# Kernel tuning notes

Hardware: AMD Instinct MI355X
Metric: run time of the kernel (lower is better)

The kernel has to match this reference:

```python
import jax, jax.numpy as jnp
import numpy as np
from jax import lax

WIRES = 4
EPS = 1e-5


def _conv2d(x, w, b):
    # x: [B,C,H,W], w: [O,I,3,3], SAME padding, stride 1
    y = lax.conv_general_dilated(x, w, (1, 1), 'SAME',
                                 dimension_numbers=('NCHW', 'OIHW', 'NCHW'))
    return y + b[None, :, None, None]


def _maxpool2(x):
    return lax.reduce_window(x, -jnp.inf, lax.max, (1, 1, 2, 2), (1, 1, 2, 2), 'VALID')


def _cnot_perm(c, t, n=WIRES):
    # wire 0 = most significant bit; CNOT is a self-inverse basis permutation
    idx = np.arange(2 ** n)
    cbit = (idx >> (n - 1 - c)) & 1
    flipped = idx ^ (1 << (n - 1 - t))
    return np.where(cbit == 1, flipped, idx)


_CNOT_PERMS = [_cnot_perm(c, c + 1) for c in range(WIRES - 1)]
_Z_SIGNS = np.stack([1.0 - 2.0 * ((np.arange(2 ** WIRES) >> (WIRES - 1 - i)) & 1)
                     for i in range(WIRES)], axis=1).astype(np.float32)  # [16, 4]


def _quantum_circuit(q_params, feats):
    # Batched state-vector sim of: RY(feats[i]) wire i; RX(params[i]) wire i;
    # CNOT chain; <Z_i>.  feats: [B,4], q_params: [4]
    hf = 0.5 * feats
    hp = 0.5 * q_params
    cy, sy = jnp.cos(hf), jnp.sin(hf)            # [B,4]
    cx, sx = jnp.cos(hp), jnp.sin(hp)            # [4]
    # per-wire state after RX @ RY |0>: amplitudes of |0>, |1>
    a0 = (cx * cy - 1j * sx * sy).astype(jnp.complex64)  # [B,4]
    a1 = (cx * sy - 1j * sx * cy).astype(jnp.complex64)  # [B,4]
    single = jnp.stack([a0, a1], axis=-1)        # [B,4,2]
    # product state -> full 16-dim state via successive outer products
    psi = single[:, 0]                           # [B,2]
    for i in range(1, WIRES):
        psi = (psi[:, :, None] * single[:, i][:, None, :]).reshape(psi.shape[0], -1)
    # CNOT chain = fixed basis permutations
    for perm in _CNOT_PERMS:
        psi = psi[:, perm]                       # [B,16]
    probs = psi.real ** 2 + psi.imag ** 2        # [B,16]
    return probs @ jnp.asarray(_Z_SIGNS)         # [B,4]


def setup_inputs() -> dict:
    key = jax.random.key(0)
    ks = jax.random.split(key, 8)
    B, C, H, W = 512, 1, 128, 128
    return {
        'x': jax.random.normal(ks[0], (B, C, H, W), jnp.float32),
        'conv1_w': jax.random.normal(ks[1], (8, C, 3, 3), jnp.float32) * 0.1,
        'conv1_b': jnp.zeros((8,), jnp.float32),
        'conv2_w': jax.random.normal(ks[2], (16, 8, 3, 3), jnp.float32) * 0.1,
        'conv2_b': jnp.zeros((16,), jnp.float32),
        'q_params': jax.random.normal(ks[3], (WIRES,), jnp.float32),
        'bn_gamma': jnp.ones((4,), jnp.float32),
        'bn_beta': jnp.zeros((4,), jnp.float32),
        'head_w': jax.random.normal(ks[4], (4, WIRES), jnp.float32) * 0.5,
        'head_b': jnp.zeros((4,), jnp.float32),
    }


def reference(x, conv1_w, conv1_b, conv2_w, conv2_b, q_params,
              bn_gamma, bn_beta, head_w, head_b):
    h = jax.nn.relu(_conv2d(x, conv1_w, conv1_b))
    h = _maxpool2(h)
    h = jax.nn.relu(_conv2d(h, conv2_w, conv2_b))
    h = _maxpool2(h)
    feats = h.mean(axis=(2, 3))                  # AdaptiveAvgPool2d(1) -> [B,16]
    q_out = _quantum_circuit(q_params, feats[:, :WIRES])  # [B,4]
    # BatchNorm1d (training mode, biased variance)
    mu = q_out.mean(axis=0)
    var = q_out.var(axis=0)
    normed = bn_gamma * (q_out - mu) / jnp.sqrt(var + EPS) + bn_beta
    return normed @ head_w.T + head_b
```

## Files before the change

### kernel.cpp

```cpp
#include <hip/hip_runtime.h>

#define EPS 1e-5f

typedef float f2 __attribute__((ext_vector_type(2)));
typedef float f4 __attribute__((ext_vector_type(4)));

__device__ __forceinline__ float uload(const float* __restrict__ p) {
  return __int_as_float(__builtin_amdgcn_readfirstlane(__float_as_int(*p)));
}

__device__ __forceinline__ f2 fma2(f2 a, f2 b, f2 c) {
  return __builtin_elementwise_fma(a, b, c);
}
__device__ __forceinline__ f2 splat2(float s) { f2 r; r.x = s; r.y = s; return r; }

__global__ __launch_bounds__(256, 4) void k12_fused(
    const float* __restrict__ x, const float* __restrict__ w1,
    const float* __restrict__ b1, const float* __restrict__ w2,
    const float* __restrict__ b2, float* __restrict__ partials) {
  __shared__ __align__(16) float p1[8][18][66];
  __shared__ float wred[4][4];

  const int q   = blockIdx.x & 3;
  const int b   = blockIdx.x >> 2;
  const int tid = threadIdx.x;
  const float* xb = x + (size_t)b * (128 * 128);

  auto c1_load = [&](int pos, float xin[4][6]) {
    const int gl = pos >> 5, i = pos & 31;
    const int G  = 16 * q - 1 + gl;
    const bool vG = ((unsigned)G) < 64u;
    const int xr0 = 2 * G - 1;
#pragma unroll
    for (int r = 0; r < 4; ++r) {
      const int row  = xr0 + r;
      const bool rok = vG && ((unsigned)row < 128u);
      const int rowc = min(max(row, 0), 127);
      const float* rp = xb + rowc * 128;
      const float le = rp[(i == 0) ? 0 : (4 * i - 1)];
      const f4 mid   = *(const f4*)(rp + 4 * i);
      const float ri = rp[(i == 31) ? 127 : (4 * i + 4)];
      xin[r][0] = (rok && i != 0)  ? le    : 0.f;
      xin[r][1] = rok              ? mid.x : 0.f;
      xin[r][2] = rok              ? mid.y : 0.f;
      xin[r][3] = rok              ? mid.z : 0.f;
      xin[r][4] = rok              ? mid.w : 0.f;
      xin[r][5] = (rok && i != 31) ? ri    : 0.f;
    }
  };
  auto c1_compute = [&](int pos, const float xin[4][6]) {
    const int gl = pos >> 5, i = pos & 31;
    const int G  = 16 * q - 1 + gl;
    const bool vG = ((unsigned)G) < 64u;
#pragma unroll 1
    for (int g = 0; g < 2; ++g) {
      f2 wpx[9][2], bias[2];
#pragma unroll
      for (int k = 0; k < 9; ++k)
#pragma unroll
        for (int p = 0; p < 2; ++p) {
          const int oc = 4 * g + 2 * p;
          f2 wv;
          wv.x = w1[oc * 9 + k];
          wv.y = w1[(oc + 1) * 9 + k];
          wpx[k][p] = wv;
        }
      bias[0].x = b1[4 * g];     bias[0].y = b1[4 * g + 1];
      bias[1].x = b1[4 * g + 2]; bias[1].y = b1[4 * g + 3];
#pragma unroll
      for (int p = 0; p < 2; ++p)
#pragma unroll
        for (int h = 0; h < 2; ++h) {
          f2 best = splat2(0.f);
#pragma unroll
          for (int dy = 0; dy < 2; ++dy)
#pragma unroll
            for (int dx = 0; dx < 2; ++dx) {
              f2 a = bias[p];
#pragma unroll
              for (int ky = 0; ky < 3; ++ky)
#pragma unroll
                for (int kx = 0; kx < 3; ++kx)
                  a = fma2(wpx[ky * 3 + kx][p],
                           splat2(xin[dy + ky][2 * h + dx + kx]), a);
              best.x = fmaxf(best.x, a.x);
              best.y = fmaxf(best.y, a.y);
            }
          const int oc0 = 4 * g + 2 * p;
          p1[oc0][gl][2 * i + 1 + h]     = vG ? best.x : 0.f;
          p1[oc0 + 1][gl][2 * i + 1 + h] = vG ? best.y : 0.f;
        }
    }
  };

  if (tid >= 96 && tid < 240) {
    int t = tid - 96;
    int ic = t / 18, r = t % 18;
    p1[ic][r][0]  = 0.f;
    p1[ic][r][65] = 0.f;
  }

  {
    float xin0[4][6];
    c1_load(tid, xin0);
    c1_compute(tid, xin0);
  }
#pragma unroll 1
  for (int pos = tid + 256; pos < 576; pos += 256) {
    float xin[4][6];
    c1_load(pos, xin);
    c1_compute(pos, xin);
  }
  __syncthreads();

  const int px2  = tid & 31;
  const int py2l = tid >> 5;

  f2 acc[2][2][2];
  {
    f2 bias0, bias1;
    bias0.x = b2[0]; bias0.y = b2[1];
    bias1.x = b2[2]; bias1.y = b2[3];
    acc[0][0][0] = bias0; acc[0][0][1] = bias0;
    acc[0][1][0] = bias0; acc[0][1][1] = bias0;
    acc[1][0][0] = bias1; acc[1][0][1] = bias1;
    acc[1][1][0] = bias1; acc[1][1][1] = bias1;
  }

  auto ld_xin = [&](int ic, float xin[4][4]) {
#pragma unroll
    for (int r = 0; r < 4; ++r) {
      const f2* rp = (const f2*)&p1[ic][2 * py2l + r][2 * px2];
      f2 v0 = rp[0], v1 = rp[1];
      xin[r][0] = v0.x; xin[r][1] = v0.y; xin[r][2] = v1.x; xin[r][3] = v1.y;
    }
  };
  auto c2_acc = [&](int ic, const float xin[4][4]) {
#pragma unroll
    for (int ky = 0; ky < 3; ++ky)
#pragma unroll
      for (int kx = 0; kx < 3; ++kx) {
        const int k = ky * 3 + kx;
        f2 wA, wB;
        wA.x = w2[0 * 72 + ic * 9 + k];
        wA.y = w2[1 * 72 + ic * 9 + k];
        wB.x = w2[2 * 72 + ic * 9 + k];
        wB.y = w2[3 * 72 + ic * 9 + k];
#pragma unroll
        for (int dy = 0; dy < 2; ++dy)
#pragma unroll
          for (int dx = 0; dx < 2; ++dx) {
            const f2 xs = splat2(xin[dy + ky][dx + kx]);
            acc[0][dy][dx] = fma2(wA, xs, acc[0][dy][dx]);
            acc[1][dy][dx] = fma2(wB, xs, acc[1][dy][dx]);
          }
      }
  };

  float xina[4][4], xinb[4][4];
  ld_xin(0, xina);
#pragma unroll 1
  for (int ic = 0; ic < 8; ic += 2) {
    ld_xin(ic + 1, xinb);
    c2_acc(ic, xina);
    if (ic < 6) ld_xin(ic + 2, xina);
    c2_acc(ic + 1, xinb);
  }

  const int lane = tid & 63, w = tid >> 6;
#pragma unroll
  for (int p = 0; p < 2; ++p) {
    f2 m01;
    m01.x = fmaxf(fmaxf(fmaxf(acc[p][0][0].x, acc[p][0][1].x),
                        fmaxf(acc[p][1][0].x, acc[p][1][1].x)), 0.f);
    m01.y = fmaxf(fmaxf(fmaxf(acc[p][0][0].y, acc[p][0][1].y),
                        fmaxf(acc[p][1][0].y, acc[p][1][1].y)), 0.f);
#pragma unroll
    for (int off = 32; off > 0; off >>= 1) {
      m01.x += __shfl_down(m01.x, off);
      m01.y += __shfl_down(m01.y, off);
    }
    if (lane == 0) { wred[w][2 * p] = m01.x; wred[w][2 * p + 1] = m01.y; }
  }
  __syncthreads();
  if (tid < 4) {
    float s = wred[0][tid] + wred[1][tid] + wred[2][tid] + wred[3][tid];
    partials[((size_t)b * 4 + q) * 4 + tid] = s;
  }
}

__global__ __launch_bounds__(512) void k3_tail(
    const float* __restrict__ partials, const float* __restrict__ qp,
    const float* __restrict__ gamma, const float* __restrict__ beta,
    const float* __restrict__ hw, const float* __restrict__ hb,
    float* __restrict__ out) {
  __shared__ float wsum[8][8];
  __shared__ float stats[8];
  const int tid = threadIdx.x;

  const f4* pp = (const f4*)(partials + tid * 16);
  f4 s0 = pp[0], s1 = pp[1], s2 = pp[2], s3 = pp[3];
  float f[4];
  f[0] = (s0.x + s1.x + s2.x + s3.x) * (1.f / 1024.f);
  f[1] = (s0.y + s1.y + s2.y + s3.y) * (1.f / 1024.f);
  f[2] = (s0.z + s1.z + s2.z + s3.z) * (1.f / 1024.f);
  f[3] = (s0.w + s1.w + s2.w + s3.w) * (1.f / 1024.f);

  float a0r[4], a0i[4], a1r[4], a1i[4];
#pragma unroll
  for (int i = 0; i < 4; ++i) {
    float cy, sy, cx, sx;
    __sincosf(0.5f * f[i], &sy, &cy);
    __sincosf(0.5f * uload(qp + i), &sx, &cx);
    a0r[i] = cx * cy; a0i[i] = -sx * sy;
    a1r[i] = cx * sy; a1i[i] = -sx * cy;
  }

  float pr[16], pi[16];
#pragma unroll
  for (int j = 0; j < 16; ++j) {
    float rr = 1.f, ii = 0.f;
#pragma unroll
    for (int w = 0; w < 4; ++w) {
      int bit = (j >> (3 - w)) & 1;
      float ar = bit ? a1r[w] : a0r[w];
      float ai = bit ? a1i[w] : a0i[w];
      float t = rr * ar - ii * ai;
      ii = rr * ai + ii * ar;
      rr = t;
    }
    pr[j] = rr; pi[j] = ii;
  }

  constexpr int comp[16] = {0, 1, 3, 2, 6, 7, 5, 4, 12, 13, 15, 14, 10, 11, 9, 8};
  float qv[4] = {0.f, 0.f, 0.f, 0.f};
#pragma unroll
  for (int j = 0; j < 16; ++j) {
    int s = comp[j];
    float p = pr[s] * pr[s] + pi[s] * pi[s];
#pragma unroll
    for (int i = 0; i < 4; ++i)
      qv[i] += ((j >> (3 - i)) & 1) ? -p : p;
  }

  float v[8];
#pragma unroll
  for (int i = 0; i < 4; ++i) { v[i] = qv[i]; v[4 + i] = qv[i] * qv[i]; }
#pragma unroll
  for (int k = 0; k < 8; ++k)
#pragma unroll
    for (int off = 32; off > 0; off >>= 1) v[k] += __shfl_down(v[k], off);
  const int lane = tid & 63, w = tid >> 6;
  if (lane == 0) {
#pragma unroll
    for (int k = 0; k < 8; ++k) wsum[w][k] = v[k];
  }
  __syncthreads();
  if (tid < 8) {
    float s = 0.f;
#pragma unroll
    for (int ww = 0; ww < 8; ++ww) s += wsum[ww][tid];
    stats[tid] = s * (1.f / 512.f);
  }
  __syncthreads();

  float nm[4];
#pragma unroll
  for (int i = 0; i < 4; ++i) {
    float mu  = stats[i];
    float var = stats[4 + i] - mu * mu;
    nm[i] = uload(gamma + i) * (qv[i] - mu) * rsqrtf(var + EPS) + uload(beta + i);
  }
#pragma unroll
  for (int k = 0; k < 4; ++k) {
    float o = uload(hb + k);
#pragma unroll
    for (int i = 0; i < 4; ++i) o = fmaf(nm[i], uload(hw + k * 4 + i), o);
    out[tid * 4 + k] = o;
  }
}

extern "C" void kernel_launch(void* const* d_in, const int* in_sizes, int n_in,
                              void* d_out, int out_size, void* d_ws, size_t ws_size,
                              hipStream_t stream) {
  const float* x  = (const float*)d_in[0];
  const float* w1 = (const float*)d_in[1];
  const float* b1 = (const float*)d_in[2];
  const float* w2 = (const float*)d_in[3];
  const float* b2 = (const float*)d_in[4];
  const float* qp = (const float*)d_in[5];
  const float* gm = (const float*)d_in[6];
  const float* bt = (const float*)d_in[7];
  const float* hw = (const float*)d_in[8];
  const float* hb = (const float*)d_in[9];
  float* out = (float*)d_out;

  float* partials = (float*)d_ws;

  k12_fused<<<512 * 4, 256, 0, stream>>>(x, w1, b1, w2, b2, partials);
  k3_tail<<<1, 512, 0, stream>>>(partials, qp, gm, bt, hw, hb, out);
}
```

Measured before the change: 117.9 us.

## Widen fused conv block to 576 threads and split conv2 channels across thread groups

The fused conv kernel now launches 576 threads per block, so each thread computes exactly one conv1 position with no second loop pass. For conv2, 512 threads are split into two groups of 256, each handling two output channels instead of four per thread, which halves per-thread accumulators and work. This adds parallelism and shortens per-thread serial work. The trade-off is larger blocks, 64 idle threads during conv2, and possibly lower occupancy now that the launch-bounds minimum-blocks hint is gone. It also reads redundant conv1 inputs.

```diff
diff --git a/kernel.cpp b/kernel.cpp
--- a/kernel.cpp
+++ b/kernel.cpp
@@ -14,12 +14,12 @@
 }
 __device__ __forceinline__ f2 splat2(float s) { f2 r; r.x = s; r.y = s; return r; }
 
-__global__ __launch_bounds__(256, 4) void k12_fused(
+__global__ __launch_bounds__(576) void k12_fused(
     const float* __restrict__ x, const float* __restrict__ w1,
     const float* __restrict__ b1, const float* __restrict__ w2,
     const float* __restrict__ b2, float* __restrict__ partials) {
   __shared__ __align__(16) float p1[8][18][66];
-  __shared__ float wred[4][4];
+  __shared__ float wred[8][2];
 
   const int q   = blockIdx.x & 3;
   const int b   = blockIdx.x >> 2;
@@ -93,6 +93,9 @@
     }
   };
 
+  float xin0[4][6];
+  c1_load(tid, xin0);
+
   if (tid >= 96 && tid < 240) {
     int t = tid - 96;
     int ic = t / 18, r = t % 18;
@@ -100,91 +103,76 @@
     p1[ic][r][65] = 0.f;
   }
 
-  {
-    float xin0[4][6];
-    c1_load(tid, xin0);
-    c1_compute(tid, xin0);
-  }
+  c1_compute(tid, xin0);
+  __syncthreads();
+
+  const int lane = tid & 63, w = tid >> 6;
+  if (tid < 512) {
+    const int px2  = tid & 31;
+    const int py2l = (tid >> 5) & 7;
+    const int g2 = __builtin_amdgcn_readfirstlane(tid >> 8);
+
+    f2 acc[2][2];
+    {
+      f2 bias;
+      bias.x = b2[2 * g2];
+      bias.y = b2[2 * g2 + 1];
+      acc[0][0] = bias; acc[0][1] = bias;
+      acc[1][0] = bias; acc[1][1] = bias;
+    }
+
+    auto ld_xin = [&](int ic, float xin[4][4]) {
+#pragma unroll
+      for (int r = 0; r < 4; ++r) {
+        const f2* rp = (const f2*)&p1[ic][2 * py2l + r][2 * px2];
+        f2 v0 = rp[0], v1 = rp[1];
+        xin[r][0] = v0.x; xin[r][1] = v0.y; xin[r][2] = v1.x; xin[r][3] = v1.y;
+      }
+    };
+    auto c2_acc = [&](int ic, const float xin[4][4]) {
+#pragma unroll
+      for (int ky = 0; ky < 3; ++ky)
+#pragma unroll
+        for (int kx = 0; kx < 3; ++kx) {
+          const int k = ky * 3 + kx;
+          f2 wp;
+          wp.x = w2[(2 * g2) * 72 + ic * 9 + k];
+          wp.y = w2[(2 * g2 + 1) * 72 + ic * 9 + k];
+#pragma unroll
+          for (int dy = 0; dy < 2; ++dy)
+#pragma unroll
+            for (int dx = 0; dx < 2; ++dx)
+              acc[dy][dx] = fma2(wp, splat2(xin[dy + ky][dx + kx]), acc[dy][dx]);
+        }
+    };
+
+    float xina[4][4], xinb[4][4];
+    ld_xin(0, xina);
 #pragma unroll 1
-  for (int pos = tid + 256; pos < 576; pos += 256) {
-    float xin[4][6];
-    c1_load(pos, xin);
-    c1_compute(pos, xin);
-  }
-  __syncthreads();
-
-  const int px2  = tid & 31;
-  const int py2l = tid >> 5;
-
-  f2 acc[2][2][2];
-  {
-    f2 bias0, bias1;
-    bias0.x = b2[0]; bias0.y = b2[1];
-    bias1.x = b2[2]; bias1.y = b2[3];
-    acc[0][0][0] = bias0; acc[0][0][1] = bias0;
-    acc[0][1][0] = bias0; acc[0][1][1] = bias0;
-    acc[1][0][0] = bias1; acc[1][0][1] = bias1;
-    acc[1][1][0] = bias1; acc[1][1][1] = bias1;
-  }
-
-  auto ld_xin = [&](int ic, float xin[4][4]) {
-#pragma unroll
-    for (int r = 0; r < 4; ++r) {
-      const f2* rp = (const f2*)&p1[ic][2 * py2l + r][2 * px2];
-      f2 v0 = rp[0], v1 = rp[1];
-      xin[r][0] = v0.x; xin[r][1] = v0.y; xin[r][2] = v1.x; xin[r][3] = v1.y;
-    }
-  };
-  auto c2_acc = [&](int ic, const float xin[4][4]) {
-#pragma unroll
-    for (int ky = 0; ky < 3; ++ky)
-#pragma unroll
-      for (int kx = 0; kx < 3; ++kx) {
-        const int k = ky * 3 + kx;
-        f2 wA, wB;
-        wA.x = w2[0 * 72 + ic * 9 + k];
-        wA.y = w2[1 * 72 + ic * 9 + k];
-        wB.x = w2[2 * 72 + ic * 9 + k];
-        wB.y = w2[3 * 72 + ic * 9 + k];
-#pragma unroll
-        for (int dy = 0; dy < 2; ++dy)
-#pragma unroll
-          for (int dx = 0; dx < 2; ++dx) {
-            const f2 xs = splat2(xin[dy + ky][dx + kx]);
-            acc[0][dy][dx] = fma2(wA, xs, acc[0][dy][dx]);
-            acc[1][dy][dx] = fma2(wB, xs, acc[1][dy][dx]);
-          }
-      }
-  };
-
-  float xina[4][4], xinb[4][4];
-  ld_xin(0, xina);
-#pragma unroll 1
-  for (int ic = 0; ic < 8; ic += 2) {
-    ld_xin(ic + 1, xinb);
-    c2_acc(ic, xina);
-    if (ic < 6) ld_xin(ic + 2, xina);
-    c2_acc(ic + 1, xinb);
-  }
-
-  const int lane = tid & 63, w = tid >> 6;
-#pragma unroll
-  for (int p = 0; p < 2; ++p) {
+    for (int ic = 0; ic < 8; ic += 2) {
+      ld_xin(ic + 1, xinb);
+      c2_acc(ic, xina);
+      if (ic < 6) ld_xin(ic + 2, xina);
+      c2_acc(ic + 1, xinb);
+    }
+
     f2 m01;
-    m01.x = fmaxf(fmaxf(fmaxf(acc[p][0][0].x, acc[p][0][1].x),
-                        fmaxf(acc[p][1][0].x, acc[p][1][1].x)), 0.f);
-    m01.y = fmaxf(fmaxf(fmaxf(acc[p][0][0].y, acc[p][0][1].y),
-                        fmaxf(acc[p][1][0].y, acc[p][1][1].y)), 0.f);
+    m01.x = fmaxf(fmaxf(fmaxf(acc[0][0].x, acc[0][1].x),
+                        fmaxf(acc[1][0].x, acc[1][1].x)), 0.f);
+    m01.y = fmaxf(fmaxf(fmaxf(acc[0][0].y, acc[0][1].y),
+                        fmaxf(acc[1][0].y, acc[1][1].y)), 0.f);
 #pragma unroll
     for (int off = 32; off > 0; off >>= 1) {
       m01.x += __shfl_down(m01.x, off);
       m01.y += __shfl_down(m01.y, off);
     }
-    if (lane == 0) { wred[w][2 * p] = m01.x; wred[w][2 * p + 1] = m01.y; }
+    if (lane == 0) { wred[w][0] = m01.x; wred[w][1] = m01.y; }
   }
   __syncthreads();
   if (tid < 4) {
-    float s = wred[0][tid] + wred[1][tid] + wred[2][tid] + wred[3][tid];
+    const int wbase = (tid >> 1) * 4, c = tid & 1;
+    float s = wred[wbase][c] + wred[wbase + 1][c] +
+              wred[wbase + 2][c] + wred[wbase + 3][c];
     partials[((size_t)b * 4 + q) * 4 + tid] = s;
   }
 }
@@ -297,6 +285,6 @@
 
   float* partials = (float*)d_ws;
 
-  k12_fused<<<512 * 4, 256, 0, stream>>>(x, w1, b1, w2, b2, partials);
+  k12_fused<<<512 * 4, 576, 0, stream>>>(x, w1, b1, w2, b2, partials);
   k3_tail<<<1, 512, 0, stream>>>(partials, qp, gm, bt, hw, hb, out);
 }
```

New measurement: 141.2 us. 19.8% more time.
